# Kernel optimization log

Hardware: AMD Instinct MI355X
Metric: run time of the kernel (lower is better)

## Reference

```python
import jax, jax.numpy as jnp
import numpy as np

N_NODES = 20000


def gcn_conv(x, src, dst, W, b, n):
    # PyG GCNConv: add self-loops, symmetric normalization, then aggregate.
    loop = jnp.arange(n, dtype=src.dtype)
    s = jnp.concatenate([src, loop])
    d = jnp.concatenate([dst, loop])
    w = jnp.ones(s.shape[0], dtype=x.dtype)
    deg = jax.ops.segment_sum(w, d, num_segments=n)  # in-degree at targets
    dinv = jnp.where(deg > 0, jax.lax.rsqrt(deg), 0.0)
    norm = dinv[s] * dinv[d]  # [E+n]
    h = x @ W  # [n, out]
    msg = h[s] * norm[:, None]  # gather + scale, [E+n, out]
    return jax.ops.segment_sum(msg, d, num_segments=n) + b


def gcn_stack(x, src, dst, W1, b1, W2, b2, n):
    h = jax.nn.relu(gcn_conv(x, src, dst, W1, b1, n))
    return gcn_conv(h, src, dst, W2, b2, n)


def setup_inputs() -> dict:
    key = jax.random.key(0)
    ks = jax.random.split(key, 12)
    n, e, din, dh, dout = N_NODES, 320000, 256, 256, 128
    x = jax.random.normal(ks[0], (n, din), dtype=jnp.float32)
    edge_index = jax.random.randint(ks[1], (2, e), 0, n, dtype=jnp.int64)
    g = lambda k, i, o: jax.random.normal(k, (i, o), dtype=jnp.float32) / np.sqrt(i)
    return {
        "x": x, "edge_index": edge_index,
        "Wf1": g(ks[2], din, dh), "bf1": jnp.zeros(dh, jnp.float32),
        "Wf2": g(ks[3], dh, dh), "bf2": jnp.zeros(dh, jnp.float32),
        "Wb1": g(ks[4], din, dh), "bb1": jnp.zeros(dh, jnp.float32),
        "Wb2": g(ks[5], dh, dh), "bb2": jnp.zeros(dh, jnp.float32),
        "Wfin": g(ks[6], 2 * dh, dout), "bfin": jnp.zeros(dout, jnp.float32),
    }


def reference(x, edge_index, Wf1, bf1, Wf2, bf2, Wb1, bb1, Wb2, bb2, Wfin, bfin):
    n = x.shape[0]
    src, dst = edge_index[0], edge_index[1]
    # forward-direction GCN stack
    x_fwd = gcn_stack(x, src, dst, Wf1, bf1, Wf2, bf2, n)
    # backward-direction GCN stack (edges reversed)
    x_bwd = gcn_stack(x, dst, src, Wb1, bb1, Wb2, bb2, n)
    x_combined = jnp.concatenate([x_fwd, x_bwd], axis=-1)  # [n, 2*hidden]
    return x_combined @ Wfin + bfin
```

## Files before the change

### kernel.cpp

```cpp
#include <hip/hip_runtime.h>

typedef unsigned int   u32;
typedef unsigned short u16;
typedef __attribute__((ext_vector_type(8))) short bf16x8;
typedef __attribute__((ext_vector_type(4))) float f32x4;

__device__ __forceinline__ u16 f2bf(float f) {
    u32 u = __float_as_uint(f);
    u32 r = u + 0x7fffu + ((u >> 16) & 1u);
    return (u16)(r >> 16);
}
__device__ __forceinline__ float bf2f(u16 h) {
    return __uint_as_float(((u32)h) << 16);
}
__device__ __forceinline__ float lof(u32 q) { return __uint_as_float(q << 16); }
__device__ __forceinline__ float hif(u32 q) { return __uint_as_float(q & 0xffff0000u); }
__device__ __forceinline__ u32 pk(float a, float b) {
    return (u32)f2bf(a) | ((u32)f2bf(b) << 16);
}
__device__ __forceinline__ void gl_lds16(const void* g, void* l) {
    __builtin_amdgcn_global_load_lds(
        (const __attribute__((address_space(1))) u32*)g,
        (__attribute__((address_space(3))) u32*)l, 16, 0, 0);
}

__global__ __launch_bounds__(256)
void k_deg(const int* __restrict__ src, const int* __restrict__ dst,
           int* __restrict__ deg_f, int* __restrict__ deg_b, int E) {
    int e = blockIdx.x * 256 + threadIdx.x;
    if (e < E) {
        atomicAdd(&deg_f[dst[e]], 1);
        atomicAdd(&deg_b[src[e]], 1);
    }
}

__global__ __launch_bounds__(256)
void k_scan1(const int* __restrict__ deg_f, const int* __restrict__ deg_b,
             float* __restrict__ dinv_f, float* __restrict__ dinv_b,
             int* __restrict__ bsum, int n, int nblk) {
    __shared__ int red[4];
    int dir = blockIdx.x >= nblk;
    int b = dir ? blockIdx.x - nblk : blockIdx.x;
    const int* deg = dir ? deg_b : deg_f;
    float* dinv = dir ? dinv_b : dinv_f;
    int idx = b * 256 + threadIdx.x;
    int d = 0;
    if (idx < n) {
        d = deg[idx];
        dinv[idx] = rsqrtf((float)(d + 1));
    }
    int s = d;
    s += __shfl_down(s, 32);
    s += __shfl_down(s, 16);
    s += __shfl_down(s, 8);
    s += __shfl_down(s, 4);
    s += __shfl_down(s, 2);
    s += __shfl_down(s, 1);
    int wv = threadIdx.x >> 6;
    if ((threadIdx.x & 63) == 0) red[wv] = s;
    __syncthreads();
    if (threadIdx.x == 0)
        bsum[blockIdx.x] = red[0] + red[1] + red[2] + red[3];
}

__global__ __launch_bounds__(256)
void k_scan2(const int* __restrict__ bsum, int* __restrict__ bpre, int nblk) {
    __shared__ int sm[256];
    int t = threadIdx.x;
    int seg = t >> 7;
    int i = t & 127;
    int val = (i < nblk) ? bsum[seg * nblk + i] : 0;
    sm[t] = val;
    __syncthreads();
    for (int s = 1; s < 128; s <<= 1) {
        int v = ((t & 127) >= s) ? sm[t - s] : 0;
        __syncthreads();
        sm[t] += v;
        __syncthreads();
    }
    if (i < nblk) bpre[seg * nblk + i] = sm[t] - val;
}

__global__ __launch_bounds__(256)
void k_scan3(const int* __restrict__ deg_f, const int* __restrict__ deg_b,
             const int* __restrict__ bpre,
             int* __restrict__ off_f, int* __restrict__ cur_f,
             int* __restrict__ off_b, int* __restrict__ cur_b,
             int n, int nblk, int E) {
    __shared__ int sm[256];
    int dir = blockIdx.x >= nblk;
    int b = dir ? blockIdx.x - nblk : blockIdx.x;
    const int* deg = dir ? deg_b : deg_f;
    int* off = dir ? off_b : off_f;
    int* cur = dir ? cur_b : cur_f;
    int base = bpre[blockIdx.x];
    int idx = b * 256 + threadIdx.x;
    int d = (idx < n) ? deg[idx] : 0;
    sm[threadIdx.x] = d;
    __syncthreads();
    for (int s = 1; s < 256; s <<= 1) {
        int v = (threadIdx.x >= s) ? sm[threadIdx.x - s] : 0;
        __syncthreads();
        sm[threadIdx.x] += v;
        __syncthreads();
    }
    if (idx < n) {
        int excl = base + sm[threadIdx.x] - d;
        off[idx] = excl;
        cur[idx] = excl;
    }
    if (blockIdx.x == 0 && threadIdx.x == 0) {
        off_f[n] = E;
        off_b[n] = E;
    }
}

__global__ __launch_bounds__(256)
void k_fill(const int* __restrict__ src, const int* __restrict__ dst,
            int* __restrict__ cur_f, int* __restrict__ cur_b,
            int* __restrict__ lst_f, int* __restrict__ lst_b, int E) {
    int e = blockIdx.x * 256 + threadIdx.x;
    if (e < E) {
        int s = src[e], d = dst[e];
        int pf = atomicAdd(&cur_f[d], 1);
        lst_f[pf] = s;
        int pb = atomicAdd(&cur_b[s], 1);
        lst_b[pb] = d;
    }
}

__global__ __launch_bounds__(256)
void k_prep(const float* __restrict__ W0, const float* __restrict__ W1,
            const float* __restrict__ W2, const float* __restrict__ W3,
            const float* __restrict__ W4,
            u16* __restrict__ h0, u16* __restrict__ l0,
            u16* __restrict__ h1, u16* __restrict__ l1,
            u16* __restrict__ h2, u16* __restrict__ l2,
            u16* __restrict__ h3, u16* __restrict__ l3,
            u16* __restrict__ h4, u16* __restrict__ l4,
            const float* __restrict__ bfin, const float* __restrict__ bf2,
            const float* __restrict__ bb2, float* __restrict__ cvec,
            const float* __restrict__ x, u16* __restrict__ xh, int xcount)
{
    __shared__ float red[256];
    int b = blockIdx.x;
    int t = threadIdx.x;
    if (b < 1280) {
        int which = b >> 8;
        int sub = ((b & 255) << 8) | t;
        const float* W; u16 *H, *L; int kshift, N;
        switch (which) {
            case 0: W = W0; H = h0; L = l0; kshift = 8; N = 256; break;
            case 1: W = W1; H = h1; L = l1; kshift = 8; N = 256; break;
            case 2: W = W2; H = h2; L = l2; kshift = 8; N = 256; break;
            case 3: W = W3; H = h3; L = l3; kshift = 8; N = 256; break;
            default: W = W4; H = h4; L = l4; kshift = 9; N = 128; break;
        }
        int ni = sub >> kshift;
        int ki = sub & ((1 << kshift) - 1);
        float v = W[(size_t)ki * N + ni];
        u16 hh = f2bf(v);
        H[sub] = hh;
        L[sub] = f2bf(v - bf2f(hh));
    } else if (b < 1408) {
        int j = b - 1280;
        float s = bf2[t] * W4[(size_t)t * 128 + j]
                + bb2[t] * W4[(size_t)(t + 256) * 128 + j];
        red[t] = s;
        __syncthreads();
        for (int st = 128; st > 0; st >>= 1) {
            if (t < st) red[t] += red[t + st];
            __syncthreads();
        }
        if (t == 0) cvec[j] = red[0] + bfin[j];
    } else {
        int i = (b - 1408) * 1024 + t * 4;
        if (i < xcount) {
            float4 v = *(const float4*)(x + i);
            ushort4 h4v;
            h4v.x = f2bf(v.x); h4v.y = f2bf(v.y);
            h4v.z = f2bf(v.z); h4v.w = f2bf(v.w);
            *(ushort4*)(xh + i) = h4v;
        }
    }
}

__global__ __launch_bounds__(256)
void k_gemm(const u16* __restrict__ A0, const u16* __restrict__ A1p,
            const u16* __restrict__ Bhi0, const u16* __restrict__ Blo0,
            const u16* __restrict__ Bhi1, const u16* __restrict__ Blo1, int ldb,
            u16* __restrict__ C0, u16* __restrict__ C1,
            const float* __restrict__ rs0, const float* __restrict__ rs1,
            int M, int N)
{
    __shared__ char smem[24576];

    const int z = blockIdx.z;
    const u16* Ah  = z ? A1p : A0;
    const u16* Bhi = z ? Bhi1 : Bhi0;
    const u16* Blo = z ? Blo1 : Blo0;
    u16* Chi       = z ? C1 : C0;
    const float* rowscale = z ? rs1 : rs0;

    const int tid  = threadIdx.x;
    const int lane = tid & 63;
    const int wid  = tid >> 6;
    const int wm   = wid >> 1, wn = wid & 1;
    const int bm   = blockIdx.x * 128;
    const int bn   = blockIdx.y * 128;

    f32x4 acc[4][4];
#pragma unroll
    for (int i = 0; i < 4; ++i)
#pragma unroll
        for (int j = 0; j < 4; ++j) acc[i][j] = (f32x4){0.f, 0.f, 0.f, 0.f};

    const int gsw  = ((lane >> 2) & 3) ^ ((lane >> 4) & 3);
    const int gsta = ((lane & 3) ^ gsw) << 4;
    const int sl   = (lane & 3) ^ ((lane >> 2) & 3);
    const int hi4  = lane >> 4;
    const int gsel = ((hi4 ^ sl) << 4);
    const int frow = lane & 15;

    for (int k0 = 0; k0 < 256; k0 += 32) {
        if (k0) __syncthreads();

#pragma unroll
        for (int p = 0; p < 2; ++p) {
            int c   = p * 4 + wid;
            int row = c * 16 + (lane >> 2);
            size_t rb = (size_t)(bn + row) * ldb + (size_t)k0 * 2 + gsta;
            gl_lds16((const char*)Bhi + rb, smem + 8192 + c * 1024);
            gl_lds16((const char*)Blo + rb, smem + 16384 + c * 1024);
        }
#pragma unroll
        for (int p = 0; p < 2; ++p) {
            int c   = p * 4 + wid;
            int row = c * 16 + (lane >> 2);
            int grow = bm + row; if (grow >= M) grow = M - 1;
            size_t rb = (size_t)grow * 512 + (size_t)k0 * 2 + gsta;
            gl_lds16((const char*)Ah + rb, smem + c * 1024);
        }
        __syncthreads();

        bf16x8 ah[4], bh[4], bl[4];
#pragma unroll
        for (int fm = 0; fm < 4; ++fm) {
            int r = wm * 64 + fm * 16 + frow;
            ah[fm] = *(const bf16x8*)(smem + r * 64 + gsel);
        }
#pragma unroll
        for (int fn = 0; fn < 4; ++fn) {
            int r = wn * 64 + fn * 16 + frow;
            bh[fn] = *(const bf16x8*)(smem + 8192 + r * 64 + gsel);
            bl[fn] = *(const bf16x8*)(smem + 16384 + r * 64 + gsel);
        }
#pragma unroll
        for (int fm = 0; fm < 4; ++fm)
#pragma unroll
            for (int fn = 0; fn < 4; ++fn)
                acc[fm][fn] = __builtin_amdgcn_mfma_f32_16x16x32_bf16(ah[fm], bh[fn], acc[fm][fn], 0, 0, 0);
#pragma unroll
        for (int fm = 0; fm < 4; ++fm)
#pragma unroll
            for (int fn = 0; fn < 4; ++fn)
                acc[fm][fn] = __builtin_amdgcn_mfma_f32_16x16x32_bf16(ah[fm], bl[fn], acc[fm][fn], 0, 0, 0);
    }

#pragma unroll
    for (int fm = 0; fm < 4; ++fm) {
#pragma unroll
        for (int q = 0; q < 4; ++q) {
            int row = bm + wm * 64 + fm * 16 + hi4 * 4 + q;
            if (row < M) {
                float s = rowscale ? rowscale[row] : 1.0f;
#pragma unroll
                for (int fn = 0; fn < 4; ++fn) {
                    int col = bn + wn * 64 + fn * 16 + frow;
                    Chi[(size_t)row * N + col] = f2bf(acc[fm][fn][q] * s);
                }
            }
        }
    }
}

__global__ __launch_bounds__(256)
void k_agg1(const u16* __restrict__ ghf, const u16* __restrict__ ghb,
            const int* __restrict__ off_f, const int* __restrict__ lst_f,
            const int* __restrict__ off_b, const int* __restrict__ lst_b,
            const float* __restrict__ dinv_f, const float* __restrict__ dinv_b,
            const float* __restrict__ b_f, const float* __restrict__ b_b,
            u16* __restrict__ ozf, u16* __restrict__ ozb, int n)
{
    int nb = gridDim.x >> 1;
    int stack = blockIdx.x >= nb;
    int bx = stack ? (blockIdx.x - nb) : blockIdx.x;
    const u16* gh = stack ? ghb : ghf;
    const int* off = stack ? off_b : off_f;
    const int* lst = stack ? lst_b : lst_f;
    const float* dinv = stack ? dinv_b : dinv_f;
    const float* bias = stack ? b_b : b_f;
    u16* oz = stack ? ozb : ozf;

    int wv = threadIdx.x >> 6;
    int half = (threadIdx.x >> 5) & 1;
    int l = threadIdx.x & 31;
    int v = bx * 8 + wv * 2 + half;
    if (v >= n) return;
    int f0 = l * 8;

    uint4 qh = *(const uint4*)(gh + (size_t)v * 256 + f0);
    float a0 = lof(qh.x), a1 = hif(qh.x);
    float a2 = lof(qh.y), a3 = hif(qh.y);
    float a4 = lof(qh.z), a5 = hif(qh.z);
    float a6 = lof(qh.w), a7 = hif(qh.w);

    int s0 = off[v], s1 = off[v + 1];
    int j = s0;
    for (; j + 8 <= s1; j += 8) {
        uint4 m[8];
#pragma unroll
        for (int q = 0; q < 8; ++q) {
            int u = lst[j + q];
            m[q] = *(const uint4*)(gh + (size_t)u * 256 + f0);
        }
#pragma unroll
        for (int q = 0; q < 8; ++q) {
            a0 += lof(m[q].x); a1 += hif(m[q].x);
            a2 += lof(m[q].y); a3 += hif(m[q].y);
            a4 += lof(m[q].z); a5 += hif(m[q].z);
            a6 += lof(m[q].w); a7 += hif(m[q].w);
        }
    }
    for (; j + 4 <= s1; j += 4) {
        uint4 m[4];
#pragma unroll
        for (int q = 0; q < 4; ++q) {
            int u = lst[j + q];
            m[q] = *(const uint4*)(gh + (size_t)u * 256 + f0);
        }
#pragma unroll
        for (int q = 0; q < 4; ++q) {
            a0 += lof(m[q].x); a1 += hif(m[q].x);
            a2 += lof(m[q].y); a3 += hif(m[q].y);
            a4 += lof(m[q].z); a5 += hif(m[q].z);
            a6 += lof(m[q].w); a7 += hif(m[q].w);
        }
    }
    for (; j < s1; ++j) {
        int u = lst[j];
        uint4 m = *(const uint4*)(gh + (size_t)u * 256 + f0);
        a0 += lof(m.x); a1 += hif(m.x);
        a2 += lof(m.y); a3 += hif(m.y);
        a4 += lof(m.z); a5 += hif(m.z);
        a6 += lof(m.w); a7 += hif(m.w);
    }
    float sc = dinv[v];
    float4 bA = *(const float4*)(bias + f0);
    float4 bB = *(const float4*)(bias + f0 + 4);
    float o0 = fmaxf(a0 * sc + bA.x, 0.f), o1 = fmaxf(a1 * sc + bA.y, 0.f);
    float o2 = fmaxf(a2 * sc + bA.z, 0.f), o3 = fmaxf(a3 * sc + bA.w, 0.f);
    float o4 = fmaxf(a4 * sc + bB.x, 0.f), o5 = fmaxf(a5 * sc + bB.y, 0.f);
    float o6 = fmaxf(a6 * sc + bB.z, 0.f), o7 = fmaxf(a7 * sc + bB.w, 0.f);
    uint4 r;
    r.x = pk(o0, o1); r.y = pk(o2, o3); r.z = pk(o4, o5); r.w = pk(o6, o7);
    *(uint4*)(oz + (size_t)v * 256 + f0) = r;
}

__global__ __launch_bounds__(256)
void k_agg2(const u16* __restrict__ yf, const u16* __restrict__ yb,
            const int* __restrict__ off_f, const int* __restrict__ lst_f,
            const int* __restrict__ off_b, const int* __restrict__ lst_b,
            const float* __restrict__ dinv_f, const float* __restrict__ dinv_b,
            const float* __restrict__ cvec, float* __restrict__ out, int n)
{
    int wv = threadIdx.x >> 6, lane = threadIdx.x & 63;
    int v = blockIdx.x * 4 + wv;
    if (v >= n) return;
    int dirb = lane >> 5;
    int l = lane & 31;
    int f0 = l * 4;

    const u16* y   = dirb ? yb : yf;
    const int* off = dirb ? off_b : off_f;
    const int* lst = dirb ? lst_b : lst_f;
    float dv = dirb ? dinv_b[v] : dinv_f[v];

    uint2 q = *(const uint2*)(y + (size_t)v * 128 + f0);
    float a0 = lof(q.x), a1 = hif(q.x), a2 = lof(q.y), a3 = hif(q.y);

    int s0 = off[v], s1 = off[v + 1];
    int j = s0;
    for (; j + 4 <= s1; j += 4) {
        int u0 = lst[j], u1 = lst[j + 1], u2 = lst[j + 2], u3 = lst[j + 3];
        uint2 m0 = *(const uint2*)(y + (size_t)u0 * 128 + f0);
        uint2 m1 = *(const uint2*)(y + (size_t)u1 * 128 + f0);
        uint2 m2 = *(const uint2*)(y + (size_t)u2 * 128 + f0);
        uint2 m3 = *(const uint2*)(y + (size_t)u3 * 128 + f0);
        a0 += lof(m0.x) + lof(m1.x) + lof(m2.x) + lof(m3.x);
        a1 += hif(m0.x) + hif(m1.x) + hif(m2.x) + hif(m3.x);
        a2 += lof(m0.y) + lof(m1.y) + lof(m2.y) + lof(m3.y);
        a3 += hif(m0.y) + hif(m1.y) + hif(m2.y) + hif(m3.y);
    }
    for (; j < s1; ++j) {
        int u = lst[j];
        uint2 m = *(const uint2*)(y + (size_t)u * 128 + f0);
        a0 += lof(m.x); a1 += hif(m.x);
        a2 += lof(m.y); a3 += hif(m.y);
    }
    float o0 = a0 * dv, o1 = a1 * dv, o2 = a2 * dv, o3 = a3 * dv;
    o0 += __shfl_xor(o0, 32);
    o1 += __shfl_xor(o1, 32);
    o2 += __shfl_xor(o2, 32);
    o3 += __shfl_xor(o3, 32);
    if (dirb == 0) {
        float4 c4 = *(const float4*)(cvec + f0);
        float4 o;
        o.x = o0 + c4.x; o.y = o1 + c4.y; o.z = o2 + c4.z; o.w = o3 + c4.w;
        *(float4*)(out + (size_t)v * 128 + f0) = o;
    }
}

extern "C" void kernel_launch(void* const* d_in, const int* in_sizes, int n_in,
                              void* d_out, int out_size, void* d_ws, size_t ws_size,
                              hipStream_t stream) {
    const float* x    = (const float*)d_in[0];
    const int*   ei   = (const int*)d_in[1];
    const float* Wf1  = (const float*)d_in[2];
    const float* bf1  = (const float*)d_in[3];
    const float* Wf2  = (const float*)d_in[4];
    const float* bf2  = (const float*)d_in[5];
    const float* Wb1  = (const float*)d_in[6];
    const float* bb1  = (const float*)d_in[7];
    const float* Wb2  = (const float*)d_in[8];
    const float* bb2  = (const float*)d_in[9];
    const float* Wfin = (const float*)d_in[10];
    const float* bfin = (const float*)d_in[11];
    float* out = (float*)d_out;

    const int n = in_sizes[0] / 256;
    const int E = in_sizes[1] / 2;
    const int* src = ei;
    const int* dst = ei + E;

    char* p = (char*)d_ws;
    auto take = [&](size_t bytes) -> void* {
        void* q = (void*)p;
        p += (bytes + 255) & ~(size_t)255;
        return q;
    };
    u16* Xh    = (u16*)take((size_t)n * 256 * 2);
    u16* P1f   = (u16*)take((size_t)n * 256 * 2);
    u16* P1b   = (u16*)take((size_t)n * 256 * 2);
    u16* Zf    = (u16*)take((size_t)n * 256 * 2);
    u16* Zb    = (u16*)take((size_t)n * 256 * 2);
    u16* H2f   = (u16*)take((size_t)n * 256 * 2);
    u16* H2b   = (u16*)take((size_t)n * 256 * 2);
    u16* Yf    = (u16*)take((size_t)n * 128 * 2);
    u16* Yb    = (u16*)take((size_t)n * 128 * 2);
    u16* w1f_h = (u16*)take(65536 * 2); u16* w1f_l = (u16*)take(65536 * 2);
    u16* w2f_h = (u16*)take(65536 * 2); u16* w2f_l = (u16*)take(65536 * 2);
    u16* w1b_h = (u16*)take(65536 * 2); u16* w1b_l = (u16*)take(65536 * 2);
    u16* w2b_h = (u16*)take(65536 * 2); u16* w2b_l = (u16*)take(65536 * 2);
    u16* wfin_h = (u16*)take(65536 * 2); u16* wfin_l = (u16*)take(65536 * 2);
    float* cvec = (float*)take(128 * sizeof(float));
    int*   deg_f  = (int*)take((size_t)n * sizeof(int));
    int*   deg_b  = (int*)take((size_t)n * sizeof(int));
    int*   off_f  = (int*)take((size_t)(n + 1) * sizeof(int));
    int*   off_b  = (int*)take((size_t)(n + 1) * sizeof(int));
    int*   cur_f  = (int*)take((size_t)n * sizeof(int));
    int*   cur_b  = (int*)take((size_t)n * sizeof(int));
    int*   lst_f  = (int*)take((size_t)E * sizeof(int));
    int*   lst_b  = (int*)take((size_t)E * sizeof(int));
    float* dinv_f = (float*)take((size_t)n * sizeof(float));
    float* dinv_b = (float*)take((size_t)n * sizeof(float));
    int*   bsum   = (int*)take(256 * sizeof(int));
    int*   bpre   = (int*)take(256 * sizeof(int));

    hipMemsetAsync(deg_f, 0, (size_t)n * sizeof(int), stream);
    hipMemsetAsync(deg_b, 0, (size_t)n * sizeof(int), stream);

    const int nblk = (n + 255) / 256;
    const int xcount = n * 256;
    const int xblocks = (xcount + 1023) / 1024;
    int eb = (E + 255) / 256;

    k_deg<<<eb, 256, 0, stream>>>(src, dst, deg_f, deg_b, E);
    k_scan1<<<2 * nblk, 256, 0, stream>>>(deg_f, deg_b, dinv_f, dinv_b, bsum, n, nblk);
    k_scan2<<<1, 256, 0, stream>>>(bsum, bpre, nblk);
    k_scan3<<<2 * nblk, 256, 0, stream>>>(deg_f, deg_b, bpre,
        off_f, cur_f, off_b, cur_b, n, nblk, E);
    k_fill<<<eb, 256, 0, stream>>>(src, dst, cur_f, cur_b, lst_f, lst_b, E);
    k_prep<<<1408 + xblocks, 256, 0, stream>>>(Wf1, Wf2, Wb1, Wb2, Wfin,
        w1f_h, w1f_l, w2f_h, w2f_l, w1b_h, w1b_l, w2b_h, w2b_l, wfin_h, wfin_l,
        bfin, bf2, bb2, cvec, x, Xh, xcount);

    const int gx = (n + 127) / 128;
    dim3 gBig(gx, 2, 2);
    dim3 gFin(gx, 1, 2);
    int ab = (n + 3) / 4;
    int a1b = 2 * ((n + 7) / 8);

    k_gemm<<<gBig, 256, 0, stream>>>(Xh, Xh,
        w1f_h, w1f_l, w1b_h, w1b_l, 512,
        P1f, P1b, dinv_f, dinv_b, n, 256);
    k_agg1<<<a1b, 256, 0, stream>>>(P1f, P1b,
        off_f, lst_f, off_b, lst_b, dinv_f, dinv_b, bf1, bb1, Zf, Zb, n);
    k_gemm<<<gBig, 256, 0, stream>>>(Zf, Zb,
        w2f_h, w2f_l, w2b_h, w2b_l, 512,
        H2f, H2b, dinv_f, dinv_b, n, 256);
    k_gemm<<<gFin, 256, 0, stream>>>(H2f, H2b,
        wfin_h, wfin_l, wfin_h + 256, wfin_l + 256, 1024,
        Yf, Yb, nullptr, nullptr, n, 128);
    k_agg2<<<ab, 256, 0, stream>>>(Yf, Yb,
        off_f, lst_f, off_b, lst_b, dinv_f, dinv_b, cvec, out, n);
}
```

Measured before the change: 279.9 us.

## Fold second-layer weights into final projection to drop one GEMM

Premultiplies W2 by the matching half of Wfin for each direction inside the prep kernel, so the layer-2 GEMM and the final GEMM become a single GEMM with N=128 applied to Z before the second aggregation. This relies on aggregation being linear, and it removes the n x 256 intermediate H2 along with one full GEMM launch. In exchange the prep kernel does a naive 256x256x128 fp32 product per direction, with strided Wfin reads, and the fused weights are rounded to split bf16 hi/lo.

Result: faster. 265.9 us (-5.0%).

```diff
diff --git a/kernel.cpp b/kernel.cpp
--- a/kernel.cpp
+++ b/kernel.cpp
@@ -130,14 +130,13 @@
 }
 
 __global__ __launch_bounds__(256)
-void k_prep(const float* __restrict__ W0, const float* __restrict__ W1,
-            const float* __restrict__ W2, const float* __restrict__ W3,
-            const float* __restrict__ W4,
-            u16* __restrict__ h0, u16* __restrict__ l0,
-            u16* __restrict__ h1, u16* __restrict__ l1,
-            u16* __restrict__ h2, u16* __restrict__ l2,
-            u16* __restrict__ h3, u16* __restrict__ l3,
-            u16* __restrict__ h4, u16* __restrict__ l4,
+void k_prep(const float* __restrict__ Wf1, const float* __restrict__ Wb1,
+            const float* __restrict__ Wf2, const float* __restrict__ Wb2,
+            const float* __restrict__ Wfin,
+            u16* __restrict__ w1f_h, u16* __restrict__ w1f_l,
+            u16* __restrict__ w1b_h, u16* __restrict__ w1b_l,
+            u16* __restrict__ wcf_h, u16* __restrict__ wcf_l,
+            u16* __restrict__ wcb_h, u16* __restrict__ wcb_l,
             const float* __restrict__ bfin, const float* __restrict__ bf2,
             const float* __restrict__ bb2, float* __restrict__ cvec,
             const float* __restrict__ x, u16* __restrict__ xh, int xcount)
@@ -145,27 +144,22 @@
     __shared__ float red[256];
     int b = blockIdx.x;
     int t = threadIdx.x;
-    if (b < 1280) {
+    if (b < 512) {
         int which = b >> 8;
         int sub = ((b & 255) << 8) | t;
-        const float* W; u16 *H, *L; int kshift, N;
-        switch (which) {
-            case 0: W = W0; H = h0; L = l0; kshift = 8; N = 256; break;
-            case 1: W = W1; H = h1; L = l1; kshift = 8; N = 256; break;
-            case 2: W = W2; H = h2; L = l2; kshift = 8; N = 256; break;
-            case 3: W = W3; H = h3; L = l3; kshift = 8; N = 256; break;
-            default: W = W4; H = h4; L = l4; kshift = 9; N = 128; break;
-        }
-        int ni = sub >> kshift;
-        int ki = sub & ((1 << kshift) - 1);
-        float v = W[(size_t)ki * N + ni];
+        const float* W = which ? Wb1 : Wf1;
+        u16* H = which ? w1b_h : w1f_h;
+        u16* L = which ? w1b_l : w1f_l;
+        int ni = sub >> 8;
+        int ki = sub & 255;
+        float v = W[(size_t)ki * 256 + ni];
         u16 hh = f2bf(v);
         H[sub] = hh;
         L[sub] = f2bf(v - bf2f(hh));
-    } else if (b < 1408) {
-        int j = b - 1280;
-        float s = bf2[t] * W4[(size_t)t * 128 + j]
-                + bb2[t] * W4[(size_t)(t + 256) * 128 + j];
+    } else if (b < 640) {
+        int j = b - 512;
+        float s = bf2[t] * Wfin[(size_t)t * 128 + j]
+                + bb2[t] * Wfin[(size_t)(t + 256) * 128 + j];
         red[t] = s;
         __syncthreads();
         for (int st = 128; st > 0; st >>= 1) {
@@ -173,8 +167,26 @@
             __syncthreads();
         }
         if (t == 0) cvec[j] = red[0] + bfin[j];
+    } else if (b < 1152) {
+        int idx = b - 640;
+        int dir = idx >> 8;
+        int i = idx & 255;
+        const float* W2 = dir ? Wb2 : Wf2;
+        u16* H = dir ? wcb_h : wcf_h;
+        u16* L = dir ? wcb_l : wcf_l;
+        if (t < 128) {
+            int j = t;
+            float s = 0.f;
+            const float* wf = Wfin + (size_t)(dir * 256) * 128 + j;
+            const float* w2r = W2 + (size_t)i * 256;
+            for (int k = 0; k < 256; ++k)
+                s += w2r[k] * wf[(size_t)k * 128];
+            u16 hh = f2bf(s);
+            H[(size_t)j * 256 + i] = hh;
+            L[(size_t)j * 256 + i] = f2bf(s - bf2f(hh));
+        }
     } else {
-        int i = (b - 1408) * 1024 + t * 4;
+        int i = (b - 1152) * 1024 + t * 4;
         if (i < xcount) {
             float4 v = *(const float4*)(x + i);
             ushort4 h4v;
@@ -454,15 +466,12 @@
     u16* P1b   = (u16*)take((size_t)n * 256 * 2);
     u16* Zf    = (u16*)take((size_t)n * 256 * 2);
     u16* Zb    = (u16*)take((size_t)n * 256 * 2);
-    u16* H2f   = (u16*)take((size_t)n * 256 * 2);
-    u16* H2b   = (u16*)take((size_t)n * 256 * 2);
     u16* Yf    = (u16*)take((size_t)n * 128 * 2);
     u16* Yb    = (u16*)take((size_t)n * 128 * 2);
     u16* w1f_h = (u16*)take(65536 * 2); u16* w1f_l = (u16*)take(65536 * 2);
-    u16* w2f_h = (u16*)take(65536 * 2); u16* w2f_l = (u16*)take(65536 * 2);
     u16* w1b_h = (u16*)take(65536 * 2); u16* w1b_l = (u16*)take(65536 * 2);
-    u16* w2b_h = (u16*)take(65536 * 2); u16* w2b_l = (u16*)take(65536 * 2);
-    u16* wfin_h = (u16*)take(65536 * 2); u16* wfin_l = (u16*)take(65536 * 2);
+    u16* wcf_h = (u16*)take(32768 * 2); u16* wcf_l = (u16*)take(32768 * 2);
+    u16* wcb_h = (u16*)take(32768 * 2); u16* wcb_l = (u16*)take(32768 * 2);
     float* cvec = (float*)take(128 * sizeof(float));
     int*   deg_f  = (int*)take((size_t)n * sizeof(int));
     int*   deg_b  = (int*)take((size_t)n * sizeof(int));
@@ -491,8 +500,8 @@
     k_scan3<<<2 * nblk, 256, 0, stream>>>(deg_f, deg_b, bpre,
         off_f, cur_f, off_b, cur_b, n, nblk, E);
     k_fill<<<eb, 256, 0, stream>>>(src, dst, cur_f, cur_b, lst_f, lst_b, E);
-    k_prep<<<1408 + xblocks, 256, 0, stream>>>(Wf1, Wf2, Wb1, Wb2, Wfin,
-        w1f_h, w1f_l, w2f_h, w2f_l, w1b_h, w1b_l, w2b_h, w2b_l, wfin_h, wfin_l,
+    k_prep<<<1152 + xblocks, 256, 0, stream>>>(Wf1, Wb1, Wf2, Wb2, Wfin,
+        w1f_h, w1f_l, w1b_h, w1b_l, wcf_h, wcf_l, wcb_h, wcb_l,
         bfin, bf2, bb2, cvec, x, Xh, xcount);
 
     const int gx = (n + 127) / 128;
@@ -506,12 +515,9 @@
         P1f, P1b, dinv_f, dinv_b, n, 256);
     k_agg1<<<a1b, 256, 0, stream>>>(P1f, P1b,
         off_f, lst_f, off_b, lst_b, dinv_f, dinv_b, bf1, bb1, Zf, Zb, n);
-    k_gemm<<<gBig, 256, 0, stream>>>(Zf, Zb,
-        w2f_h, w2f_l, w2b_h, w2b_l, 512,
-        H2f, H2b, dinv_f, dinv_b, n, 256);
-    k_gemm<<<gFin, 256, 0, stream>>>(H2f, H2b,
-        wfin_h, wfin_l, wfin_h + 256, wfin_l + 256, 1024,
-        Yf, Yb, nullptr, nullptr, n, 128);
+    k_gemm<<<gFin, 256, 0, stream>>>(Zf, Zb,
+        wcf_h, wcf_l, wcb_h, wcb_l, 512,
+        Yf, Yb, dinv_f, dinv_b, n, 128);
     k_agg2<<<ab, 256, 0, stream>>>(Yf, Yb,
         off_f, lst_f, off_b, lst_b, dinv_f, dinv_b, cvec, out, n);
 }
```
